# Performance work log

Hardware: AMD Instinct MI355X
Metric: run time of the kernel (lower is better)

The kernel has to match this reference:

```python
import jax, jax.numpy as jnp
import numpy as np
import math

B, S, D = 2, 2048, 2048
H, KV, HD = 32, 8, 64
G = H // KV  # 4
BASE = 10000.0


def _rope_tables(seq_len, dtype):
    inv_freq = 1.0 / (BASE ** (jnp.arange(0, HD, 2, dtype=jnp.float32) / HD))
    t = jnp.arange(seq_len, dtype=jnp.float32)
    freqs = jnp.outer(t, inv_freq)               # [S, HD/2]
    emb = jnp.concatenate([freqs, freqs], -1)     # [S, HD]
    return jnp.cos(emb).astype(dtype), jnp.sin(emb).astype(dtype)


def _rotate_half(x):
    x1, x2 = x[..., : HD // 2], x[..., HD // 2 :]
    return jnp.concatenate([-x2, x1], axis=-1)


def setup_inputs() -> dict:
    key = jax.random.key(0)
    ks = jax.random.split(key, 5)
    s = 0.02
    return {
        "hidden_states": jax.random.normal(ks[0], (B, S, D), jnp.float32),
        "Wq": jax.random.normal(ks[1], (D, H * HD), jnp.float32) * s,
        "Wk": jax.random.normal(ks[2], (D, KV * HD), jnp.float32) * s,
        "Wv": jax.random.normal(ks[3], (D, KV * HD), jnp.float32) * s,
        "Wo": jax.random.normal(ks[4], (D, D), jnp.float32) * s,
    }


def reference(hidden_states, Wq, Wk, Wv, Wo):
    b, s, _ = hidden_states.shape
    q = (hidden_states @ Wq).reshape(b, s, H, HD).transpose(0, 2, 1, 3)   # [B,H,S,HD]
    k = (hidden_states @ Wk).reshape(b, s, KV, HD).transpose(0, 2, 1, 3)  # [B,KV,S,HD]
    v = (hidden_states @ Wv).reshape(b, s, KV, HD).transpose(0, 2, 1, 3)

    cos, sin = _rope_tables(s, hidden_states.dtype)  # [S, HD]
    cos = cos[None, None]
    sin = sin[None, None]
    q = q * cos + _rotate_half(q) * sin
    k = k * cos + _rotate_half(k) * sin

    # GQA: repeat kv heads to match query heads
    k = jnp.repeat(k, G, axis=1)  # [B,H,S,HD]
    v = jnp.repeat(v, G, axis=1)

    scores = jnp.einsum("bhqd,bhkd->bhqk", q, k) / math.sqrt(HD)
    causal = jnp.triu(jnp.full((s, s), float("-inf"), dtype=scores.dtype), k=1)
    scores = scores + causal
    attn = jax.nn.softmax(scores, axis=-1)
    out = jnp.einsum("bhqk,bhkd->bhqd", attn, v)          # [B,H,S,HD]
    out = out.transpose(0, 2, 1, 3).reshape(b, s, H * HD)  # [B,S,D]
    return out @ Wo
```

## Files before the change

### kernel.cpp

```cpp
#include <hip/hip_runtime.h>
#include <hip/hip_bf16.h>

#define BATCH  2
#define SEQ    2048
#define DMODEL 2048
#define NHEADS 32
#define NKV    8
#define HDIM   64
#define ROWS   (BATCH * SEQ)
#define NQKV   3072

typedef __attribute__((ext_vector_type(8))) short bf16x8;
typedef __attribute__((ext_vector_type(4))) float floatx4;

__device__ __forceinline__ float b2f(unsigned short u) {
    union { unsigned int i; float f; } x; x.i = ((unsigned int)u) << 16; return x.f;
}
__device__ __forceinline__ unsigned short f2b(float f) {
    union { float f; unsigned int i; } x; x.f = f;
    unsigned int r = x.i + 0x7fffu + ((x.i >> 16) & 1u);
    return (unsigned short)(r >> 16);
}
__device__ __forceinline__ unsigned int pkbf(float a, float b) {
    union { __hip_bfloat162 h; unsigned int u; } x;
    x.h = __float22bfloat162_rn(make_float2(a, b));
    return x.u;
}

#define GLD16(g, l) __builtin_amdgcn_global_load_lds( \
    (const __attribute__((address_space(1))) unsigned int*)(g), \
    (__attribute__((address_space(3))) unsigned int*)(l), 16, 0, 0)

template <bool BF16_OUT>
__global__ __launch_bounds__(256) void mfma_gemm(const unsigned short* __restrict__ A,
                                                 const unsigned short* __restrict__ Bt,
                                                 void* __restrict__ Cout,
                                                 int M, int N, int K) {
    __shared__ unsigned short As[128 * 32];
    __shared__ unsigned short Bs[128 * 32];

    const int tid  = threadIdx.x;
    const int wave = tid >> 6;
    const int lane = tid & 63;
    const int m0 = blockIdx.y * 128;
    const int n0 = blockIdx.x * 128;
    const int wr0 = (wave >> 1) * 64;
    const int wc0 = (wave & 1) * 64;

    const int srow = wave * 32 + (lane >> 2);
    const int skc  = (lane & 3) * 8;
    const unsigned short* Ap0 = A  + (size_t)(m0 + srow) * K + skc;
    const unsigned short* Ap1 = Ap0 + (size_t)16 * K;
    const unsigned short* Bp0 = Bt + (size_t)(n0 + srow) * K + skc;
    const unsigned short* Bp1 = Bp0 + (size_t)16 * K;
    unsigned short* Al0 = &As[wave * 1024];
    unsigned short* Al1 = &As[wave * 1024 + 512];
    unsigned short* Bl0 = &Bs[wave * 1024];
    unsigned short* Bl1 = &Bs[wave * 1024 + 512];

    const int fr = lane & 15;
    const int fk = (lane >> 4) * 8;

    floatx4 acc[4][4];
    #pragma unroll
    for (int r = 0; r < 4; ++r)
        #pragma unroll
        for (int c = 0; c < 4; ++c)
            #pragma unroll
            for (int g = 0; g < 4; ++g) acc[r][c][g] = 0.f;

    for (int k0 = 0; k0 < K; k0 += 32) {
        __syncthreads();
        GLD16(Ap0 + k0, Al0);
        GLD16(Ap1 + k0, Al1);
        GLD16(Bp0 + k0, Bl0);
        GLD16(Bp1 + k0, Bl1);
        __syncthreads();

        bf16x8 af[4], bfr[4];
        #pragma unroll
        for (int r = 0; r < 4; ++r)
            af[r] = *(const bf16x8*)&As[(wr0 + r * 16 + fr) * 32 + fk];
        #pragma unroll
        for (int c = 0; c < 4; ++c)
            bfr[c] = *(const bf16x8*)&Bs[(wc0 + c * 16 + fr) * 32 + fk];
        #pragma unroll
        for (int r = 0; r < 4; ++r)
            #pragma unroll
            for (int c = 0; c < 4; ++c)
                acc[r][c] = __builtin_amdgcn_mfma_f32_16x16x32_bf16(af[r], bfr[c], acc[r][c], 0, 0, 0);
    }

    const int erow = (lane >> 4) * 4;
    const int ecol = lane & 15;
    #pragma unroll
    for (int r = 0; r < 4; ++r)
        #pragma unroll
        for (int c = 0; c < 4; ++c)
            #pragma unroll
            for (int g = 0; g < 4; ++g) {
                int row = m0 + wr0 + r * 16 + erow + g;
                int col = n0 + wc0 + c * 16 + ecol;
                if (BF16_OUT)
                    ((unsigned short*)Cout)[(size_t)row * N + col] = f2b(acc[r][c][g]);
                else
                    ((float*)Cout)[(size_t)row * N + col] = acc[r][c][g];
            }
}

__global__ __launch_bounds__(256) void transpose_cast_all(const float* __restrict__ Wq,
                                                          const float* __restrict__ Wk,
                                                          const float* __restrict__ Wv,
                                                          const float* __restrict__ Wo,
                                                          unsigned short* __restrict__ Wt,
                                                          unsigned short* __restrict__ Wot) {
    __shared__ float t[32][33];
    int bx = blockIdx.x;
    const float* src; unsigned short* dst; int N, nb;
    if (bx < 64)      { src = Wq; dst = Wt;                          N = 2048; nb = bx; }
    else if (bx < 80) { src = Wk; dst = Wt + (size_t)2048 * DMODEL;  N = 512;  nb = bx - 64; }
    else if (bx < 96) { src = Wv; dst = Wt + (size_t)2560 * DMODEL;  N = 512;  nb = bx - 80; }
    else              { src = Wo; dst = Wot;                         N = 2048; nb = bx - 96; }
    const int n0 = nb * 32, k0 = blockIdx.y * 32;
    const int tx = threadIdx.x & 31, ty = threadIdx.x >> 5;
    #pragma unroll
    for (int i = 0; i < 32; i += 8)
        t[ty + i][tx] = src[(size_t)(k0 + ty + i) * N + n0 + tx];
    __syncthreads();
    #pragma unroll
    for (int i = 0; i < 32; i += 8)
        dst[(size_t)(n0 + ty + i) * DMODEL + k0 + tx] = f2b(t[tx][ty + i]);
}

__global__ void cast_f32_to_bf16(const float* __restrict__ src,
                                 unsigned short* __restrict__ dst, int n) {
    int i = (blockIdx.x * 256 + threadIdx.x) * 8;
    if (i >= n) return;
    float4 a = *(const float4*)(src + i);
    float4 b = *(const float4*)(src + i + 4);
    uint4 o;
    o.x = pkbf(a.x, a.y); o.y = pkbf(a.z, a.w);
    o.z = pkbf(b.x, b.y); o.w = pkbf(b.z, b.w);
    *(uint4*)(dst + i) = o;
}

__global__ void rope_all(unsigned short* __restrict__ buf) {
    int idx = blockIdx.x * blockDim.x + threadIdx.x;
    int i   = idx & 31;
    int tmp = idx >> 5;
    int hh  = tmp % 40;
    int row = tmp / 40;
    if (row >= ROWS) return;
    float scale = (hh < 32) ? 0.125f : 1.0f;
    int t = row & (SEQ - 1);
    float inv_freq = powf(10000.0f, -(float)i * (1.0f / 32.0f));
    float ang = (float)t * inv_freq;
    float s, c;
    sincosf(ang, &s, &c);
    unsigned short* p = buf + (size_t)row * NQKV + hh * 64 + i;
    float x1 = b2f(p[0]), x2 = b2f(p[32]);
    p[0]  = f2b((x1 * c - x2 * s) * scale);
    p[32] = f2b((x2 * c + x1 * s) * scale);
}

__global__ __launch_bounds__(256, 4) void attn_mfma(const unsigned short* __restrict__ QKV,
                                                    unsigned short* __restrict__ Ctx) {
    __shared__ unsigned short Ks[64][72];
    __shared__ unsigned short Vts[64][72];
    __shared__ unsigned short Ps[4][32][72];

    const int tid  = threadIdx.x;
    const int wave = tid >> 6;
    const int lane = tid & 63;
    const int px = blockIdx.x;
    const int h  = blockIdx.y;
    const int b  = blockIdx.z;
    const int kvh = h >> 2;

    const int fr = lane & 15;
    const int fg = lane >> 4;
    const size_t base = (size_t)(b * SEQ) * NQKV;

    const int krow = tid >> 2, kc0 = (tid & 3) * 16;
    const int vp2 = tid & 31, vh0 = (tid >> 5) * 8;
    const unsigned short* kbase = QKV + base + (size_t)krow * NQKV + 2048 + kvh * HDIM + kc0;
    const unsigned short* vbase = QKV + base + (size_t)(2 * vp2) * NQKV + 2560 + kvh * HDIM + vh0;

    const int qb = 15 - px;
    const int wbase = qb * 128 + wave * 32;

    bf16x8 qf[2][2];
    #pragma unroll
    for (int rg = 0; rg < 2; ++rg)
        #pragma unroll
        for (int ks = 0; ks < 2; ++ks)
            qf[rg][ks] = *(const bf16x8*)(QKV + base + (size_t)(wbase + rg * 16 + fr) * NQKV
                                          + h * HDIM + ks * 32 + fg * 8);

    float l[2];
    floatx4 acc[4][2];
    #pragma unroll
    for (int rg = 0; rg < 2; ++rg) l[rg] = 0.f;
    #pragma unroll
    for (int j2 = 0; j2 < 4; ++j2)
        #pragma unroll
        for (int rg = 0; rg < 2; ++rg)
            #pragma unroll
            for (int g = 0; g < 4; ++g) acc[j2][rg][g] = 0.f;

    const int nkb = 2 * qb + 2;

    bf16x8 kr0 = *(const bf16x8*)kbase;
    bf16x8 kr1 = *(const bf16x8*)(kbase + 8);
    bf16x8 v0  = *(const bf16x8*)vbase;
    bf16x8 v1  = *(const bf16x8*)(vbase + NQKV);

    for (int kb = 0; kb < nkb; ++kb) {
        __syncthreads();
        *(bf16x8*)&Ks[krow][kc0]     = kr0;
        *(bf16x8*)&Ks[krow][kc0 + 8] = kr1;
        #pragma unroll
        for (int j = 0; j < 8; ++j) {
            unsigned int w = (unsigned int)(unsigned short)v0[j]
                           | ((unsigned int)(unsigned short)v1[j] << 16);
            *(unsigned int*)&Vts[vh0 + j][2 * vp2] = w;
        }
        {
            int nx = (kb + 1 < nkb) ? kb + 1 : kb;
            const unsigned short* kp = kbase + (size_t)(nx * 64) * NQKV;
            const unsigned short* vp = vbase + (size_t)(nx * 64) * NQKV;
            kr0 = *(const bf16x8*)kp;
            kr1 = *(const bf16x8*)(kp + 8);
            v0  = *(const bf16x8*)vp;
            v1  = *(const bf16x8*)(vp + NQKV);
        }
        __syncthreads();

        const bool skip = (kb * 64 > wbase + 31);
        if (!skip) {
            const bool needMask = (kb * 64 + 63 > wbase);

            floatx4 sc[4][2];
            #pragma unroll
            for (int j = 0; j < 4; ++j)
                #pragma unroll
                for (int rg = 0; rg < 2; ++rg)
                    #pragma unroll
                    for (int g = 0; g < 4; ++g) sc[j][rg][g] = 0.f;
            __builtin_amdgcn_s_setprio(1);
            #pragma unroll
            for (int ks = 0; ks < 2; ++ks) {
                #pragma unroll
                for (int j = 0; j < 4; ++j) {
                    bf16x8 kf = *(const bf16x8*)&Ks[j * 16 + fr][ks * 32 + fg * 8];
                    #pragma unroll
                    for (int rg = 0; rg < 2; ++rg)
                        sc[j][rg] = __builtin_amdgcn_mfma_f32_16x16x32_bf16(kf, qf[rg][ks], sc[j][rg], 0, 0, 0);
                }
            }
            __builtin_amdgcn_s_setprio(0);

            if (needMask) {
                #pragma unroll
                for (int rg = 0; rg < 2; ++rg) {
                    int qi = wbase + rg * 16 + fr;
                    #pragma unroll
                    for (int j = 0; j < 4; ++j)
                        #pragma unroll
                        for (int g = 0; g < 4; ++g) {
                            int kj = kb * 64 + j * 16 + fg * 4 + g;
                            if (kj > qi) sc[j][rg][g] = -1e30f;
                        }
                }
            }

            #pragma unroll
            for (int rg = 0; rg < 2; ++rg) {
                #pragma unroll
                for (int j = 0; j < 4; ++j) {
                    #pragma unroll
                    for (int g = 0; g < 4; ++g) {
                        float e = __expf(sc[j][rg][g]);
                        sc[j][rg][g] = e;
                        l[rg] += e;
                    }
                    uint2 w;
                    w.x = pkbf(sc[j][rg][0], sc[j][rg][1]);
                    w.y = pkbf(sc[j][rg][2], sc[j][rg][3]);
                    *(uint2*)&Ps[wave][rg * 16 + fr][j * 16 + fg * 4] = w;
                }
            }

            __builtin_amdgcn_s_setprio(1);
            #pragma unroll
            for (int ks = 0; ks < 2; ++ks) {
                bf16x8 pf[2];
                #pragma unroll
                for (int rg = 0; rg < 2; ++rg)
                    pf[rg] = *(const bf16x8*)&Ps[wave][rg * 16 + fr][ks * 32 + fg * 8];
                #pragma unroll
                for (int j2 = 0; j2 < 4; ++j2) {
                    bf16x8 vf = *(const bf16x8*)&Vts[j2 * 16 + fr][ks * 32 + fg * 8];
                    #pragma unroll
                    for (int rg = 0; rg < 2; ++rg)
                        acc[j2][rg] = __builtin_amdgcn_mfma_f32_16x16x32_bf16(vf, pf[rg], acc[j2][rg], 0, 0, 0);
                }
            }
            __builtin_amdgcn_s_setprio(0);
        }
    }

    #pragma unroll
    for (int rg = 0; rg < 2; ++rg) {
        float lt = l[rg];
        lt += __shfl_xor(lt, 16);
        lt += __shfl_xor(lt, 32);
        float inv = 1.0f / lt;
        int q = wbase + rg * 16 + fr;
        unsigned short* cp = Ctx + (size_t)(b * SEQ + q) * DMODEL + h * HDIM;
        #pragma unroll
        for (int j2 = 0; j2 < 4; ++j2) {
            uint2 w;
            w.x = pkbf(acc[j2][rg][0] * inv, acc[j2][rg][1] * inv);
            w.y = pkbf(acc[j2][rg][2] * inv, acc[j2][rg][3] * inv);
            *(uint2*)(cp + j2 * 16 + fg * 4) = w;
        }
    }
}

extern "C" void kernel_launch(void* const* d_in, const int* in_sizes, int n_in,
                              void* d_out, int out_size, void* d_ws, size_t ws_size,
                              hipStream_t stream) {
    const float* X  = (const float*)d_in[0];
    const float* Wq = (const float*)d_in[1];
    const float* Wk = (const float*)d_in[2];
    const float* Wv = (const float*)d_in[3];
    const float* Wo = (const float*)d_in[4];
    float* out = (float*)d_out;

    unsigned short* Xb   = (unsigned short*)d_ws;
    unsigned short* Wt   = Xb + (size_t)ROWS * DMODEL;
    unsigned short* Wot  = Wt + (size_t)NQKV * DMODEL;
    unsigned short* QKVb = Wot + (size_t)DMODEL * DMODEL;
    unsigned short* Ctxb = QKVb + (size_t)ROWS * NQKV;

    cast_f32_to_bf16<<<(ROWS * DMODEL) / (8 * 256), 256, 0, stream>>>(X, Xb, ROWS * DMODEL);
    transpose_cast_all<<<dim3(160, 64), 256, 0, stream>>>(Wq, Wk, Wv, Wo, Wt, Wot);

    mfma_gemm<true><<<dim3(NQKV / 128, ROWS / 128), 256, 0, stream>>>(Xb, Wt, QKVb, ROWS, NQKV, DMODEL);

    rope_all<<<(ROWS * 40 * 32) / 256, 256, 0, stream>>>(QKVb);

    attn_mfma<<<dim3(SEQ / 128, NHEADS, BATCH), 256, 0, stream>>>(QKVb, Ctxb);

    mfma_gemm<false><<<dim3(DMODEL / 128, ROWS / 128), 256, 0, stream>>>(Ctxb, Wot, out, ROWS, DMODEL, DMODEL);
}
```

Measured before the change: 368.6 us.

## Balance causal attention by pairing short and long query tiles per block

The attention kernel now uses 128-thread blocks covering 64 query rows, and each block processes two query tiles (31-px and px) in sequence, so every block does roughly equal causal work. This removes the load imbalance of the old scheme, where blocks near the diagonal start finished early and long blocks dominated the tail. The cost is more global K/V traffic per wave, since each staged K/V tile is now shared by 2 waves instead of 4, plus a serialized second pass. Launch bounds and staging loops are adjusted to match the smaller block.

New measurement: 331.0 us. -10.2%, faster.

```diff
diff --git a/kernel.cpp b/kernel.cpp
--- a/kernel.cpp
+++ b/kernel.cpp
@@ -163,11 +163,11 @@
     p[32] = f2b((x2 * c + x1 * s) * scale);
 }
 
-__global__ __launch_bounds__(256, 4) void attn_mfma(const unsigned short* __restrict__ QKV,
+__global__ __launch_bounds__(128, 3) void attn_mfma(const unsigned short* __restrict__ QKV,
                                                     unsigned short* __restrict__ Ctx) {
     __shared__ unsigned short Ks[64][72];
     __shared__ unsigned short Vts[64][72];
-    __shared__ unsigned short Ps[4][32][72];
+    __shared__ unsigned short Ps[2][32][72];
 
     const int tid  = threadIdx.x;
     const int wave = tid >> 6;
@@ -181,149 +181,162 @@
     const int fg = lane >> 4;
     const size_t base = (size_t)(b * SEQ) * NQKV;
 
-    const int krow = tid >> 2, kc0 = (tid & 3) * 16;
-    const int vp2 = tid & 31, vh0 = (tid >> 5) * 8;
+    const int krow = tid >> 1, kc0 = (tid & 1) * 32;
+    const int vp2 = tid & 31, vh0 = (tid >> 5) * 16;
     const unsigned short* kbase = QKV + base + (size_t)krow * NQKV + 2048 + kvh * HDIM + kc0;
     const unsigned short* vbase = QKV + base + (size_t)(2 * vp2) * NQKV + 2560 + kvh * HDIM + vh0;
 
-    const int qb = 15 - px;
-    const int wbase = qb * 128 + wave * 32;
-
-    bf16x8 qf[2][2];
-    #pragma unroll
-    for (int rg = 0; rg < 2; ++rg)
-        #pragma unroll
-        for (int ks = 0; ks < 2; ++ks)
-            qf[rg][ks] = *(const bf16x8*)(QKV + base + (size_t)(wbase + rg * 16 + fr) * NQKV
-                                          + h * HDIM + ks * 32 + fg * 8);
-
-    float l[2];
-    floatx4 acc[4][2];
-    #pragma unroll
-    for (int rg = 0; rg < 2; ++rg) l[rg] = 0.f;
-    #pragma unroll
-    for (int j2 = 0; j2 < 4; ++j2)
+    #pragma unroll 1
+    for (int t = 0; t < 2; ++t) {
+        const int qb = (t == 0) ? (31 - px) : px;
+        const int wbase = qb * 64 + wave * 32;
+
+        bf16x8 qf[2][2];
         #pragma unroll
         for (int rg = 0; rg < 2; ++rg)
             #pragma unroll
-            for (int g = 0; g < 4; ++g) acc[j2][rg][g] = 0.f;
-
-    const int nkb = 2 * qb + 2;
-
-    bf16x8 kr0 = *(const bf16x8*)kbase;
-    bf16x8 kr1 = *(const bf16x8*)(kbase + 8);
-    bf16x8 v0  = *(const bf16x8*)vbase;
-    bf16x8 v1  = *(const bf16x8*)(vbase + NQKV);
-
-    for (int kb = 0; kb < nkb; ++kb) {
-        __syncthreads();
-        *(bf16x8*)&Ks[krow][kc0]     = kr0;
-        *(bf16x8*)&Ks[krow][kc0 + 8] = kr1;
-        #pragma unroll
-        for (int j = 0; j < 8; ++j) {
-            unsigned int w = (unsigned int)(unsigned short)v0[j]
-                           | ((unsigned int)(unsigned short)v1[j] << 16);
-            *(unsigned int*)&Vts[vh0 + j][2 * vp2] = w;
+            for (int ks = 0; ks < 2; ++ks)
+                qf[rg][ks] = *(const bf16x8*)(QKV + base + (size_t)(wbase + rg * 16 + fr) * NQKV
+                                              + h * HDIM + ks * 32 + fg * 8);
+
+        float l[2];
+        floatx4 acc[4][2];
+        #pragma unroll
+        for (int rg = 0; rg < 2; ++rg) l[rg] = 0.f;
+        #pragma unroll
+        for (int j2 = 0; j2 < 4; ++j2)
+            #pragma unroll
+            for (int rg = 0; rg < 2; ++rg)
+                #pragma unroll
+                for (int g = 0; g < 4; ++g) acc[j2][rg][g] = 0.f;
+
+        const int nkb = qb + 1;
+
+        bf16x8 kr[4], va[2], vb[2];
+        #pragma unroll
+        for (int j = 0; j < 4; ++j) kr[j] = *(const bf16x8*)(kbase + 8 * j);
+        #pragma unroll
+        for (int j = 0; j < 2; ++j) {
+            va[j] = *(const bf16x8*)(vbase + 8 * j);
+            vb[j] = *(const bf16x8*)(vbase + NQKV + 8 * j);
         }
-        {
-            int nx = (kb + 1 < nkb) ? kb + 1 : kb;
-            const unsigned short* kp = kbase + (size_t)(nx * 64) * NQKV;
-            const unsigned short* vp = vbase + (size_t)(nx * 64) * NQKV;
-            kr0 = *(const bf16x8*)kp;
-            kr1 = *(const bf16x8*)(kp + 8);
-            v0  = *(const bf16x8*)vp;
-            v1  = *(const bf16x8*)(vp + NQKV);
+
+        for (int kb = 0; kb < nkb; ++kb) {
+            __syncthreads();
+            #pragma unroll
+            for (int j = 0; j < 4; ++j)
+                *(bf16x8*)&Ks[krow][kc0 + 8 * j] = kr[j];
+            #pragma unroll
+            for (int jj = 0; jj < 2; ++jj)
+                #pragma unroll
+                for (int j = 0; j < 8; ++j) {
+                    unsigned int w = (unsigned int)(unsigned short)va[jj][j]
+                                   | ((unsigned int)(unsigned short)vb[jj][j] << 16);
+                    *(unsigned int*)&Vts[vh0 + jj * 8 + j][2 * vp2] = w;
+                }
+            {
+                int nx = (kb + 1 < nkb) ? kb + 1 : kb;
+                const unsigned short* kp = kbase + (size_t)(nx * 64) * NQKV;
+                const unsigned short* vp = vbase + (size_t)(nx * 64) * NQKV;
+                #pragma unroll
+                for (int j = 0; j < 4; ++j) kr[j] = *(const bf16x8*)(kp + 8 * j);
+                #pragma unroll
+                for (int j = 0; j < 2; ++j) {
+                    va[j] = *(const bf16x8*)(vp + 8 * j);
+                    vb[j] = *(const bf16x8*)(vp + NQKV + 8 * j);
+                }
+            }
+            __syncthreads();
+
+            const bool skip = (kb * 64 > wbase + 31);
+            if (!skip) {
+                const bool needMask = (kb * 64 + 63 > wbase);
+
+                floatx4 sc[4][2];
+                #pragma unroll
+                for (int j = 0; j < 4; ++j)
+                    #pragma unroll
+                    for (int rg = 0; rg < 2; ++rg)
+                        #pragma unroll
+                        for (int g = 0; g < 4; ++g) sc[j][rg][g] = 0.f;
+                __builtin_amdgcn_s_setprio(1);
+                #pragma unroll
+                for (int ks = 0; ks < 2; ++ks) {
+                    #pragma unroll
+                    for (int j = 0; j < 4; ++j) {
+                        bf16x8 kf = *(const bf16x8*)&Ks[j * 16 + fr][ks * 32 + fg * 8];
+                        #pragma unroll
+                        for (int rg = 0; rg < 2; ++rg)
+                            sc[j][rg] = __builtin_amdgcn_mfma_f32_16x16x32_bf16(kf, qf[rg][ks], sc[j][rg], 0, 0, 0);
+                    }
+                }
+                __builtin_amdgcn_s_setprio(0);
+
+                if (needMask) {
+                    #pragma unroll
+                    for (int rg = 0; rg < 2; ++rg) {
+                        int qi = wbase + rg * 16 + fr;
+                        #pragma unroll
+                        for (int j = 0; j < 4; ++j)
+                            #pragma unroll
+                            for (int g = 0; g < 4; ++g) {
+                                int kj = kb * 64 + j * 16 + fg * 4 + g;
+                                if (kj > qi) sc[j][rg][g] = -1e30f;
+                            }
+                    }
+                }
+
+                #pragma unroll
+                for (int rg = 0; rg < 2; ++rg) {
+                    #pragma unroll
+                    for (int j = 0; j < 4; ++j) {
+                        #pragma unroll
+                        for (int g = 0; g < 4; ++g) {
+                            float e = __expf(sc[j][rg][g]);
+                            sc[j][rg][g] = e;
+                            l[rg] += e;
+                        }
+                        uint2 w;
+                        w.x = pkbf(sc[j][rg][0], sc[j][rg][1]);
+                        w.y = pkbf(sc[j][rg][2], sc[j][rg][3]);
+                        *(uint2*)&Ps[wave][rg * 16 + fr][j * 16 + fg * 4] = w;
+                    }
+                }
+
+                __builtin_amdgcn_s_setprio(1);
+                #pragma unroll
+                for (int ks = 0; ks < 2; ++ks) {
+                    bf16x8 pf[2];
+                    #pragma unroll
+                    for (int rg = 0; rg < 2; ++rg)
+                        pf[rg] = *(const bf16x8*)&Ps[wave][rg * 16 + fr][ks * 32 + fg * 8];
+                    #pragma unroll
+                    for (int j2 = 0; j2 < 4; ++j2) {
+                        bf16x8 vf = *(const bf16x8*)&Vts[j2 * 16 + fr][ks * 32 + fg * 8];
+                        #pragma unroll
+                        for (int rg = 0; rg < 2; ++rg)
+                            acc[j2][rg] = __builtin_amdgcn_mfma_f32_16x16x32_bf16(vf, pf[rg], acc[j2][rg], 0, 0, 0);
+                    }
+                }
+                __builtin_amdgcn_s_setprio(0);
+            }
         }
-        __syncthreads();
-
-        const bool skip = (kb * 64 > wbase + 31);
-        if (!skip) {
-            const bool needMask = (kb * 64 + 63 > wbase);
-
-            floatx4 sc[4][2];
-            #pragma unroll
-            for (int j = 0; j < 4; ++j)
-                #pragma unroll
-                for (int rg = 0; rg < 2; ++rg)
-                    #pragma unroll
-                    for (int g = 0; g < 4; ++g) sc[j][rg][g] = 0.f;
-            __builtin_amdgcn_s_setprio(1);
-            #pragma unroll
-            for (int ks = 0; ks < 2; ++ks) {
-                #pragma unroll
-                for (int j = 0; j < 4; ++j) {
-                    bf16x8 kf = *(const bf16x8*)&Ks[j * 16 + fr][ks * 32 + fg * 8];
-                    #pragma unroll
-                    for (int rg = 0; rg < 2; ++rg)
-                        sc[j][rg] = __builtin_amdgcn_mfma_f32_16x16x32_bf16(kf, qf[rg][ks], sc[j][rg], 0, 0, 0);
-                }
+
+        #pragma unroll
+        for (int rg = 0; rg < 2; ++rg) {
+            float lt = l[rg];
+            lt += __shfl_xor(lt, 16);
+            lt += __shfl_xor(lt, 32);
+            float inv = 1.0f / lt;
+            int q = wbase + rg * 16 + fr;
+            unsigned short* cp = Ctx + (size_t)(b * SEQ + q) * DMODEL + h * HDIM;
+            #pragma unroll
+            for (int j2 = 0; j2 < 4; ++j2) {
+                uint2 w;
+                w.x = pkbf(acc[j2][rg][0] * inv, acc[j2][rg][1] * inv);
+                w.y = pkbf(acc[j2][rg][2] * inv, acc[j2][rg][3] * inv);
+                *(uint2*)(cp + j2 * 16 + fg * 4) = w;
             }
-            __builtin_amdgcn_s_setprio(0);
-
-            if (needMask) {
-                #pragma unroll
-                for (int rg = 0; rg < 2; ++rg) {
-                    int qi = wbase + rg * 16 + fr;
-                    #pragma unroll
-                    for (int j = 0; j < 4; ++j)
-                        #pragma unroll
-                        for (int g = 0; g < 4; ++g) {
-                            int kj = kb * 64 + j * 16 + fg * 4 + g;
-                            if (kj > qi) sc[j][rg][g] = -1e30f;
-                        }
-                }
-            }
-
-            #pragma unroll
-            for (int rg = 0; rg < 2; ++rg) {
-                #pragma unroll
-                for (int j = 0; j < 4; ++j) {
-                    #pragma unroll
-                    for (int g = 0; g < 4; ++g) {
-                        float e = __expf(sc[j][rg][g]);
-                        sc[j][rg][g] = e;
-                        l[rg] += e;
-                    }
-                    uint2 w;
-                    w.x = pkbf(sc[j][rg][0], sc[j][rg][1]);
-                    w.y = pkbf(sc[j][rg][2], sc[j][rg][3]);
-                    *(uint2*)&Ps[wave][rg * 16 + fr][j * 16 + fg * 4] = w;
-                }
-            }
-
-            __builtin_amdgcn_s_setprio(1);
-            #pragma unroll
-            for (int ks = 0; ks < 2; ++ks) {
-                bf16x8 pf[2];
-                #pragma unroll
-                for (int rg = 0; rg < 2; ++rg)
-                    pf[rg] = *(const bf16x8*)&Ps[wave][rg * 16 + fr][ks * 32 + fg * 8];
-                #pragma unroll
-                for (int j2 = 0; j2 < 4; ++j2) {
-                    bf16x8 vf = *(const bf16x8*)&Vts[j2 * 16 + fr][ks * 32 + fg * 8];
-                    #pragma unroll
-                    for (int rg = 0; rg < 2; ++rg)
-                        acc[j2][rg] = __builtin_amdgcn_mfma_f32_16x16x32_bf16(vf, pf[rg], acc[j2][rg], 0, 0, 0);
-                }
-            }
-            __builtin_amdgcn_s_setprio(0);
-        }
-    }
-
-    #pragma unroll
-    for (int rg = 0; rg < 2; ++rg) {
-        float lt = l[rg];
-        lt += __shfl_xor(lt, 16);
-        lt += __shfl_xor(lt, 32);
-        float inv = 1.0f / lt;
-        int q = wbase + rg * 16 + fr;
-        unsigned short* cp = Ctx + (size_t)(b * SEQ + q) * DMODEL + h * HDIM;
-        #pragma unroll
-        for (int j2 = 0; j2 < 4; ++j2) {
-            uint2 w;
-            w.x = pkbf(acc[j2][rg][0] * inv, acc[j2][rg][1] * inv);
-            w.y = pkbf(acc[j2][rg][2] * inv, acc[j2][rg][3] * inv);
-            *(uint2*)(cp + j2 * 16 + fg * 4) = w;
         }
     }
 }
@@ -351,7 +364,7 @@
 
     rope_all<<<(ROWS * 40 * 32) / 256, 256, 0, stream>>>(QKVb);
 
-    attn_mfma<<<dim3(SEQ / 128, NHEADS, BATCH), 256, 0, stream>>>(QKVb, Ctxb);
+    attn_mfma<<<dim3(16, NHEADS, BATCH), 128, 0, stream>>>(QKVb, Ctxb);
 
     mfma_gemm<false><<<dim3(DMODEL / 128, ROWS / 128), 256, 0, stream>>>(Ctxb, Wot, out, ROWS, DMODEL, DMODEL);
 }
```
